# Kernel optimization log

Measured on AMD Instinct MI355X. Metric: run time of the kernel, lower is better.

## Reference

```python
import jax, jax.numpy as jnp
import numpy as np

DIM = 1024
NUM_HEAVY = 1024
N_ITERS = 50
EPS = 1.0
FETCH_K_RATIO = 9.0 / 8.0


def rms_norm(x, gamma):
    # F.normalize(x, dim=-1) * sqrt(d) * gamma
    norm = jnp.maximum(jnp.linalg.norm(x, axis=-1, keepdims=True), 1e-12)
    return (x / norm) * (x.shape[-1] ** 0.5) * gamma


def feed_forward(x, gamma, w1, b1, w2, b2):
    h = jax.nn.gelu(rms_norm(x, gamma) @ w1 + b1, approximate=False)
    return h @ w2 + b2


def coor_descent(s, k, n_iters, eps):
    # Wright et al. coordinate descent routing scores (eps_decay=1 -> constant eps)
    logk = jnp.log(jnp.asarray(k, dtype=s.dtype))

    def step(ab, _):
        a, b = ab
        sb = (s + b) / eps
        a = eps * (logk - jax.scipy.special.logsumexp(sb, axis=-1, keepdims=True))
        b = -jax.nn.relu(s + a)
        return (a, b), None

    a0 = jnp.zeros_like(s[..., :1])
    b0 = -s
    (a, b), _ = jax.lax.scan(step, (a0, b0), None, length=n_iters)
    return jnp.exp((s + a + b) / eps)


def setup_inputs() -> dict:
    key = jax.random.key(0)
    ks = jax.random.split(key, 8)
    b, n, d = 4, 8192, DIM
    dl, dh = int(d * 0.5), d * 4
    u = lambda k, shape, fan_in: jax.random.uniform(k, shape, jnp.float32, -1.0, 1.0) / np.sqrt(fan_in)
    return {
        "x": jax.random.normal(ks[0], (b, n, d), jnp.float32),
        "routing_token": jax.random.normal(ks[1], (d,), jnp.float32),
        "light_gamma": jnp.ones((d,), jnp.float32),
        "light_w1": u(ks[2], (d, dl), d),
        "light_b1": jnp.zeros((dl,), jnp.float32),
        "light_w2": u(ks[3], (dl, d), dl),
        "light_b2": jnp.zeros((d,), jnp.float32),
        "heavy_gamma": jnp.ones((d,), jnp.float32),
        "heavy_w1": u(ks[4], (d, dh), d),
        "heavy_b1": jnp.zeros((dh,), jnp.float32),
        "heavy_w2": u(ks[5], (dh, d), dh),
        "heavy_b2": jnp.zeros((d,), jnp.float32),
    }


def reference(x, routing_token, light_gamma, light_w1, light_b1, light_w2, light_b2,
              heavy_gamma, heavy_w1, heavy_b1, heavy_w2, heavy_b2):
    b, n, d = x.shape
    # light branch over all tokens
    light_out = feed_forward(x, light_gamma, light_w1, light_b1, light_w2, light_b2)

    # coordinate-descent router (single routing token)
    s = jnp.einsum('bnd,d->bn', x, routing_token)
    effective_k = min(NUM_HEAVY * FETCH_K_RATIO, n)
    scores = coor_descent(s, effective_k, N_ITERS, EPS)
    sel_scores, sel_idx = jax.lax.top_k(scores, NUM_HEAVY)  # [b, k]
    # straight-through: forward value 1.0, gradient flows through sel_scores
    sel_scores = sel_scores + jax.lax.stop_gradient(1.0 - sel_scores)

    # gather -> heavy FFN -> scale -> scatter back
    routed = jnp.take_along_axis(x, sel_idx[..., None], axis=1)  # [b, k, d]
    routed_out = feed_forward(routed, heavy_gamma, heavy_w1, heavy_b1, heavy_w2, heavy_b2)
    routed_out = routed_out * sel_scores[..., None]
    batch_idx = jnp.arange(b)[:, None]
    heavy_out = jnp.zeros_like(x).at[batch_idx, sel_idx].set(routed_out)

    return light_out + heavy_out
```

## Files before the change

kernel.cpp:

```cpp
#include <hip/hip_runtime.h>
#include <hip/hip_bf16.h>
#include <math.h>

#define DIMD   1024
#define NBATCH 4
#define NSEQ   8192
#define NTOK   (NBATCH * NSEQ)
#define NHEAVY 1024
#define NSEL   (NBATCH * NHEAVY)
#define DLIGHT 512
#define DHEAVY 4096
#define NITERS 50
#define BK     64

typedef __attribute__((ext_vector_type(8))) short short8;
typedef __attribute__((ext_vector_type(4))) float f32x4;
typedef __attribute__((ext_vector_type(4))) unsigned short u16x4;

__device__ __forceinline__ unsigned short f2bf(float f) {
    __hip_bfloat16 h = __float2bfloat16(f);
    union { __hip_bfloat16 h; unsigned short u; } cvt;
    cvt.h = h;
    return cvt.u;
}

__device__ __forceinline__ float bf2f(unsigned short u) {
    return __uint_as_float((unsigned)u << 16);
}

__device__ __forceinline__ float gelu_fast(float x) {
    float ax = fabsf(x) * 0.7071067811865475f;
    float t = 1.0f / fmaf(0.3275911f, ax, 1.0f);
    float p = fmaf(t, 1.061405429f, -1.453152027f);
    p = fmaf(t, p, 1.421413741f);
    p = fmaf(t, p, -0.284496736f);
    p = fmaf(t, p, 0.254829592f);
    p = p * t;
    float e = __expf(-ax * ax);
    float erf_abs = fmaf(-p, e, 1.0f);
    float erf = copysignf(erf_abs, x);
    return 0.5f * x * (1.0f + erf);
}

__device__ __forceinline__ void gload_lds16(const void* g, void* l) {
    __builtin_amdgcn_global_load_lds(
        (const __attribute__((address_space(1))) void*)g,
        (__attribute__((address_space(3))) void*)l,
        16, 0, 0);
}

__global__ __launch_bounds__(256) void fused_init(
    const float* __restrict__ lw1, const float* __restrict__ lw2,
    const float* __restrict__ hw1, const float* __restrict__ hw2,
    const float* __restrict__ lgamma, const float* __restrict__ hgamma,
    short* __restrict__ wl1t, short* __restrict__ wl2t,
    short* __restrict__ wh1t, short* __restrict__ wh2t,
    const float* __restrict__ x, const float* __restrict__ rt,
    unsigned short* __restrict__ xb, float* __restrict__ sc,
    double* __restrict__ s_out) {
    __shared__ float tile[32][33];
    __shared__ float red[4];
    __shared__ double redd[4];
    int b = blockIdx.x;
    int tid = threadIdx.x;

    const float* cin = nullptr; short* cout = nullptr; const float* cg = nullptr;
    int cK = 0, cN = 0, cnx = 0, cb = 0;
    if (b < 512)        { cin = lw1; cout = wl1t; cg = lgamma; cK = DIMD;   cN = DLIGHT; cnx = 16;  cb = b; }
    else if (b < 1024)  { cin = lw2; cout = wl2t; cg = nullptr; cK = DLIGHT; cN = DIMD;  cnx = 32;  cb = b - 512; }
    else if (b < 5120)  { cin = hw1; cout = wh1t; cg = hgamma; cK = DIMD;   cN = DHEAVY; cnx = 128; cb = b - 1024; }
    else if (b < 9216)  { cin = hw2; cout = wh2t; cg = nullptr; cK = DHEAVY; cN = DIMD;  cnx = 32;  cb = b - 5120; }

    if (cin) {
        int n0 = (cb % cnx) * 32, k0 = (cb / cnx) * 32;
        int tx = tid & 31, ty = tid >> 5;
        #pragma unroll
        for (int j = 0; j < 4; j++) {
            int k = k0 + ty + 8 * j;
            float g = cg ? cg[k] : 1.0f;
            tile[ty + 8 * j][tx] = cin[(size_t)k * cN + (n0 + tx)] * g;
        }
        __syncthreads();
        #pragma unroll
        for (int j = 0; j < 4; j++)
            cout[(size_t)(n0 + ty + 8 * j) * cK + (k0 + tx)] =
                (short)f2bf(tile[tx][ty + 8 * j]);
        return;
    }

    int t = b - 9216;
    const float4* xr = (const float4*)(x + (size_t)t * DIMD);
    float4 v = xr[tid];
    ushort4 pk;
    pk.x = f2bf(v.x); pk.y = f2bf(v.y); pk.z = f2bf(v.z); pk.w = f2bf(v.w);
    ((ushort4*)(xb + (size_t)t * DIMD))[tid] = pk;

    float ss = v.x * v.x + v.y * v.y + v.z * v.z + v.w * v.w;
    float4 rv = ((const float4*)rt)[tid];
    double sd = (double)v.x * rv.x + (double)v.y * rv.y + (double)v.z * rv.z + (double)v.w * rv.w;
    #pragma unroll
    for (int off = 32; off > 0; off >>= 1) {
        ss += __shfl_down(ss, off);
        sd += __shfl_down(sd, off);
    }
    if ((tid & 63) == 0) { red[tid >> 6] = ss; redd[tid >> 6] = sd; }
    __syncthreads();
    if (tid == 0) {
        s_out[t] = redd[0] + redd[1] + redd[2] + redd[3];
        float tot = red[0] + red[1] + red[2] + red[3];
        sc[t] = 32.0f / fmaxf(sqrtf(tot), 1e-12f);
    }
}

__global__ void descent_kern(const double* __restrict__ s, double* __restrict__ a_out) {
    int r = blockIdx.x, tid = threadIdx.x;
    const double* sr = s + (size_t)r * NSEQ;
    double es[8];
    #pragma unroll
    for (int i = 0; i < 8; i++) es[i] = exp(sr[tid + i * 1024]);
    __shared__ double red[2][16];
    const double Kk = 1152.0;
    double ea = exp(log(Kk) - log((double)NSEQ));
    for (int it = 1; it < NITERS; it++) {
        double loc = 0.0;
        #pragma unroll
        for (int i = 0; i < 8; i++) {
            double p = es[i] * ea;
            loc += (p < 1.0 ? p : 1.0);
        }
        #pragma unroll
        for (int off = 32; off > 0; off >>= 1) loc += __shfl_down(loc, off);
        int pb = it & 1;
        if ((tid & 63) == 0) red[pb][tid >> 6] = loc;
        __syncthreads();
        double S = 0.0;
        #pragma unroll
        for (int i = 0; i < 16; i++) S += red[pb][i];
        ea = ea * (Kk / S);
    }
    if (tid == 0) a_out[r] = log(ea);
}

__global__ void select_kern(const double* __restrict__ s, const double* __restrict__ a_arr,
                            int* __restrict__ sel, int* __restrict__ inv) {
    int r = blockIdx.x, l = threadIdx.x;
    const double* sr = s + (size_t)r * NSEQ;
    double a = a_arr[r];
    __shared__ double sw[NSEQ];
    int cnt = 0;
    for (int base = 0; base < NSEQ; base += 64) {
        int idx = base + l;
        double v = sr[idx];
        bool sat = (v + a) >= 0.0;
        sw[idx] = sat ? -1.0e300 : v;
        unsigned long long m = __ballot(sat);
        int pre = __popcll(m & ((1ull << l) - 1ull));
        if (sat) {
            int slot = cnt + pre;
            if (slot < NHEAVY) {
                sel[r * NHEAVY + slot] = r * NSEQ + idx;
                inv[r * NSEQ + idx] = r * NHEAVY + slot;
            }
        }
        cnt += (int)__popcll(m);
    }
    __syncthreads();
    for (int slot = cnt; slot < NHEAVY; slot++) {
        double best = -1.0e301; int bidx = NSEQ;
        for (int i = 0; i < NSEQ / 64; i++) {
            int idx = i * 64 + l;
            double v = sw[idx];
            if (v > best) { best = v; bidx = idx; }
        }
        #pragma unroll
        for (int off = 32; off > 0; off >>= 1) {
            double ov = __shfl_down(best, off);
            int oi = __shfl_down(bidx, off);
            if (ov > best || (ov == best && oi < bidx)) { best = ov; bidx = oi; }
        }
        bidx = __shfl(bidx, 0);
        if (l == 0) {
            sel[r * NHEAVY + slot] = r * NSEQ + bidx;
            inv[r * NSEQ + bidx] = r * NHEAVY + slot;
            sw[bidx] = -1.0e300;
        }
        __syncthreads();
    }
}

__global__ __launch_bounds__(256) void reduce_hv_kern(
    const unsigned short* __restrict__ phb, const float* __restrict__ hb2,
    float* __restrict__ hv, int nsk) {
    int h = blockIdx.x;
    int c0 = threadIdx.x * 4;
    f32x4 acc = *reinterpret_cast<const f32x4*>(hb2 + c0);
    for (int j = 0; j < nsk; j++) {
        u16x4 p = *reinterpret_cast<const u16x4*>(phb + ((size_t)j * NSEL + h) * DIMD + c0);
        #pragma unroll
        for (int rg = 0; rg < 4; rg++) acc[rg] += bf2f(p[rg]);
    }
    *reinterpret_cast<f32x4*>(hv + (size_t)h * DIMD + c0) = acc;
}

template <int EPI, bool GATHER>
__global__ __launch_bounds__(512) void gemm256(
    const short* __restrict__ A, const short* __restrict__ Bt,
    const float* __restrict__ bias,
    const float* __restrict__ sc, const int* __restrict__ sel,
    const int* __restrict__ inv, const float* __restrict__ hv,
    float* __restrict__ outf, __hip_bfloat16* __restrict__ outb,
    int M, int N, int K) {
    __shared__ alignas(16) short As[2][2][128 * 64];
    __shared__ alignas(16) short Bs[2][2][128 * 64];

    int nx = gridDim.x, ny = gridDim.y;
    int nwg = nx * ny * gridDim.z;
    int id = ((int)blockIdx.z * ny + blockIdx.y) * nx + blockIdx.x;
    if ((nwg & 7) == 0) id = (id & 7) * (nwg >> 3) + (id >> 3);
    int bxi = id % nx; int rem = id / nx;
    int byi = rem % ny; int bz = rem / ny;
    int klen = K / (int)gridDim.z, k0base = bz * klen;
    int bn0 = bxi * 256, bm0 = byi * 256;

    int tid = threadIdx.x;
    int l = tid & 63, w = tid >> 6;
    int wr = w >> 2, wc = w & 3;

    f32x4 zero = {0.f, 0.f, 0.f, 0.f};
    f32x4 acc[8][4];
    #pragma unroll
    for (int i = 0; i < 8; i++)
        #pragma unroll
        for (int j = 0; j < 4; j++) acc[i][j] = zero;

    const short* aSrc[2][2];
    const short* bSrc[2][2];
    #pragma unroll
    for (int h = 0; h < 2; h++)
        #pragma unroll
        for (int j = 0; j < 2; j++) {
            int p = j * 8192 + tid * 16;
            int o = p ^ (((p >> 7) & 7) << 4);
            int lrow = o >> 7, colb = o & 127;
            int agrow = bm0 + h * 128 + lrow;
            int garow = GATHER ? sel[agrow] : agrow;
            aSrc[h][j] = A + (size_t)garow * K + (colb >> 1);
            bSrc[h][j] = Bt + (size_t)(bn0 + h * 128 + lrow) * K + (colb >> 1);
        }

    auto stageA = [&](int b, int h, int kof) {
        #pragma unroll
        for (int j = 0; j < 2; j++)
            gload_lds16(aSrc[h][j] + kof, &As[b][h][j * 4096 + w * 512]);
    };
    auto stageB = [&](int b, int h, int kof) {
        #pragma unroll
        for (int j = 0; j < 2; j++)
            gload_lds16(bSrc[h][j] + kof, &Bs[b][h][j * 4096 + w * 512]);
    };

    int nt = klen / BK;
    stageA(0, 0, k0base); stageA(0, 1, k0base);
    stageB(0, 0, k0base); stageB(0, 1, k0base);
    if (nt > 1) {
        stageB(1, 0, k0base + BK); stageB(1, 1, k0base + BK);
        asm volatile("s_waitcnt vmcnt(4)" ::: "memory");
    } else {
        asm volatile("s_waitcnt vmcnt(0)" ::: "memory");
    }
    __builtin_amdgcn_s_barrier();

    const int lr = l & 15;
    const int swz = (lr & 7) << 4;
    const int rbase = lr * 128;
    const int colk[2] = { (((l >> 4) * 16)) ^ swz, (((l >> 4) * 16) + 64) ^ swz };

    short8 bfr[4][2];
    for (int t = 0; t < nt; ++t) {
        int d = t & 1;
        const char* aHalf = (const char*)(&As[d][wr][0]);
        const char* bHalf = (const char*)(&Bs[d][wc >> 1][0]) + (wc & 1) * 8192;
        #pragma unroll
        for (int q = 0; q < 4; q++) {
            if (q == 0) {
                #pragma unroll
                for (int ni = 0; ni < 4; ni++)
                    #pragma unroll
                    for (int kk = 0; kk < 2; kk++)
                        bfr[ni][kk] = *reinterpret_cast<const short8*>(bHalf + rbase + ni * 2048 + colk[kk]);
            }
            short8 afr[2][2];
            #pragma unroll
            for (int m2 = 0; m2 < 2; m2++)
                #pragma unroll
                for (int kk = 0; kk < 2; kk++)
                    afr[m2][kk] = *reinterpret_cast<const short8*>(aHalf + rbase + (q * 2 + m2) * 2048 + colk[kk]);
            if (q == 0 && t + 1 < nt) stageA(d ^ 1, 0, k0base + (t + 1) * BK);
            else if (q == 1 && t + 1 < nt) stageA(d ^ 1, 1, k0base + (t + 1) * BK);
            else if (q == 2 && t + 2 < nt) stageB(d, 0, k0base + (t + 2) * BK);
            else if (q == 3 && t + 2 < nt) stageB(d, 1, k0base + (t + 2) * BK);
            if (q == 3) {
                if (t + 2 < nt) asm volatile("s_waitcnt vmcnt(4)" ::: "memory");
                else            asm volatile("s_waitcnt vmcnt(0)" ::: "memory");
            }
            __builtin_amdgcn_s_barrier();
            asm volatile("s_waitcnt lgkmcnt(0)" ::: "memory");
            __builtin_amdgcn_sched_barrier(0);
            __builtin_amdgcn_s_setprio(1);
            #pragma unroll
            for (int m2 = 0; m2 < 2; m2++)
                #pragma unroll
                for (int ni = 0; ni < 4; ni++)
                    #pragma unroll
                    for (int kk = 0; kk < 2; kk++)
                        acc[q * 2 + m2][ni] = __builtin_amdgcn_mfma_f32_16x16x32_bf16(
                            bfr[ni][kk], afr[m2][kk], acc[q * 2 + m2][ni], 0, 0, 0);
            __builtin_amdgcn_s_setprio(0);
            __builtin_amdgcn_s_barrier();
        }
    }

    int orow0 = bm0 + wr * 128, ocol0 = bn0 + wc * 64;
    const int lq = (l >> 4) * 4;
    #pragma unroll
    for (int mi = 0; mi < 8; mi++) {
        int row = orow0 + mi * 16 + lr;
        float scv = 0.0f;
        int iv = -1;
        if (EPI == 0) scv = sc[GATHER ? sel[row] : row];
        if (EPI == 3) iv = inv[row];
        #pragma unroll
        for (int ni = 0; ni < 4; ni++) {
            int c0 = ocol0 + ni * 16 + lq;
            if (EPI == 0) {
                f32x4 bv = *reinterpret_cast<const f32x4*>(bias + c0);
                u16x4 pk;
                #pragma unroll
                for (int rg = 0; rg < 4; rg++)
                    pk[rg] = f2bf(gelu_fast(fmaf(scv, acc[mi][ni][rg], bv[rg])));
                *reinterpret_cast<u16x4*>((unsigned short*)outb + (size_t)row * N + c0) = pk;
            } else if (EPI == 2) {
                u16x4 pk;
                #pragma unroll
                for (int rg = 0; rg < 4; rg++) pk[rg] = f2bf(acc[mi][ni][rg]);
                *reinterpret_cast<u16x4*>((unsigned short*)outb + ((size_t)bz * M + row) * (size_t)N + c0) = pk;
            } else {
                f32x4 bv = *reinterpret_cast<const f32x4*>(bias + c0);
                f32x4 v = acc[mi][ni] + bv;
                if (iv >= 0) {
                    f32x4 hvv = *reinterpret_cast<const f32x4*>(hv + (size_t)iv * DIMD + c0);
                    v = v + hvv;
                }
                *reinterpret_cast<f32x4*>(outf + (size_t)row * N + c0) = v;
            }
        }
    }
}

extern "C" void kernel_launch(void* const* d_in, const int* in_sizes, int n_in,
                              void* d_out, int out_size, void* d_ws, size_t ws_size,
                              hipStream_t stream) {
    (void)in_sizes; (void)n_in; (void)out_size;
    const float* x      = (const float*)d_in[0];
    const float* rt     = (const float*)d_in[1];
    const float* lgamma = (const float*)d_in[2];
    const float* lw1    = (const float*)d_in[3];
    const float* lb1    = (const float*)d_in[4];
    const float* lw2    = (const float*)d_in[5];
    const float* lb2    = (const float*)d_in[6];
    const float* hgamma = (const float*)d_in[7];
    const float* hw1    = (const float*)d_in[8];
    const float* hb1    = (const float*)d_in[9];
    const float* hw2    = (const float*)d_in[10];
    const float* hb2    = (const float*)d_in[11];
    float* out = (float*)d_out;

    auto rnd = [](size_t b) { return (b + 255) & ~(size_t)255; };
    size_t fixed = rnd(NTOK * sizeof(double))
                 + rnd(256)
                 + rnd(NSEL * sizeof(int))
                 + rnd(NTOK * sizeof(int))
                 + rnd(NTOK * sizeof(float))
                 + rnd((size_t)DLIGHT * DIMD * 2)
                 + rnd((size_t)DIMD * DLIGHT * 2)
                 + rnd((size_t)DHEAVY * DIMD * 2)
                 + rnd((size_t)DIMD * DHEAVY * 2)
                 + rnd((size_t)NTOK * DIMD * 2)
                 + rnd((size_t)NSEL * DHEAVY * 2)
                 + rnd((size_t)NSEL * DIMD * 4);
    int nsk = 4;
    while (nsk > 1 && fixed + rnd((size_t)nsk * NSEL * DIMD * 2) > ws_size) nsk >>= 1;

    char* base = (char*)d_ws;
    size_t off = 0;
    auto alloc = [&](size_t bytes) -> void* {
        void* p = base + off;
        off += rnd(bytes);
        return p;
    };
    double* s     = (double*)alloc(NTOK * sizeof(double));
    double* a_arr = (double*)alloc(256);
    int*    sel   = (int*)alloc(NSEL * sizeof(int));
    int*    inv   = (int*)alloc(NTOK * sizeof(int));
    float*  sc    = (float*)alloc(NTOK * sizeof(float));
    short*  wl1t  = (short*)alloc((size_t)DLIGHT * DIMD * 2);
    short*  wl2t  = (short*)alloc((size_t)DIMD * DLIGHT * 2);
    short*  wh1t  = (short*)alloc((size_t)DHEAVY * DIMD * 2);
    short*  wh2t  = (short*)alloc((size_t)DIMD * DHEAVY * 2);
    short*  xb    = (short*)alloc((size_t)NTOK * DIMD * 2);
    short*  hh    = (short*)alloc((size_t)NSEL * DHEAVY * 2);
    float*  hv    = (float*)alloc((size_t)NSEL * DIMD * 4);
    short*  hl    = hh;
    short*  phb   = (short*)alloc((size_t)nsk * NSEL * DIMD * 2);

    hipMemsetAsync(inv, 0xFF, NTOK * sizeof(int), stream);

    fused_init<<<9216 + NTOK, 256, 0, stream>>>(
        lw1, lw2, hw1, hw2, lgamma, hgamma,
        wl1t, wl2t, wh1t, wh2t,
        x, rt, (unsigned short*)xb, sc, s);

    descent_kern<<<NBATCH, 1024, 0, stream>>>(s, a_arr);
    select_kern<<<NBATCH, 64, 0, stream>>>(s, a_arr, sel, inv);

    gemm256<0, true><<<dim3(DHEAVY / 256, NSEL / 256), 512, 0, stream>>>(
        xb, wh1t, hb1, sc, sel, nullptr, nullptr,
        nullptr, (__hip_bfloat16*)hh, NSEL, DHEAVY, DIMD);
    gemm256<2, false><<<dim3(DIMD / 256, NSEL / 256, nsk), 512, 0, stream>>>(
        hh, wh2t, nullptr, nullptr, nullptr, nullptr, nullptr,
        nullptr, (__hip_bfloat16*)phb, NSEL, DIMD, DHEAVY);
    reduce_hv_kern<<<NSEL, 256, 0, stream>>>((const unsigned short*)phb, hb2, hv, nsk);

    gemm256<0, false><<<dim3(DLIGHT / 256, NTOK / 256), 512, 0, stream>>>(
        xb, wl1t, lb1, sc, nullptr, nullptr, nullptr,
        nullptr, (__hip_bfloat16*)hl, NTOK, DLIGHT, DIMD);
    gemm256<3, false><<<dim3(DIMD / 256, NTOK / 256), 512, 0, stream>>>(
        hl, wl2t, lb2, nullptr, nullptr, inv, hv,
        out, nullptr, NTOK, DIMD, DLIGHT);
}
```

Baseline: 357.8 us.

## Overlap serial coordinate-descent router with light FFN first GEMM in one launch

Replaces the standalone 4-block descent kernel with a combined kernel whose first 4 blocks run the router iterations while the remaining 1024 blocks compute the light-branch first GEMM (128x128 tiles, GELU epilogue). The latency-bound 50-iteration descent, which used only 4 blocks, should then hide behind useful GEMM work. The light hidden buffer moves to its own allocation instead of aliasing the heavy hidden buffer, and the final output store becomes nontemporal. Risks: the smaller 128-tile GEMM may be less efficient than the 256-tile version, the descent blocks now use 256 threads with 32 values each, and the workspace grows.

```diff
diff --git a/kernel.cpp b/kernel.cpp
--- a/kernel.cpp
+++ b/kernel.cpp
@@ -112,33 +112,129 @@
     }
 }
 
-__global__ void descent_kern(const double* __restrict__ s, double* __restrict__ a_out) {
-    int r = blockIdx.x, tid = threadIdx.x;
-    const double* sr = s + (size_t)r * NSEQ;
-    double es[8];
-    #pragma unroll
-    for (int i = 0; i < 8; i++) es[i] = exp(sr[tid + i * 1024]);
-    __shared__ double red[2][16];
-    const double Kk = 1152.0;
-    double ea = exp(log(Kk) - log((double)NSEQ));
-    for (int it = 1; it < NITERS; it++) {
-        double loc = 0.0;
-        #pragma unroll
-        for (int i = 0; i < 8; i++) {
-            double p = es[i] * ea;
-            loc += (p < 1.0 ? p : 1.0);
-        }
-        #pragma unroll
-        for (int off = 32; off > 0; off >>= 1) loc += __shfl_down(loc, off);
-        int pb = it & 1;
-        if ((tid & 63) == 0) red[pb][tid >> 6] = loc;
-        __syncthreads();
-        double S = 0.0;
-        #pragma unroll
-        for (int i = 0; i < 16; i++) S += red[pb][i];
-        ea = ea * (Kk / S);
-    }
-    if (tid == 0) a_out[r] = log(ea);
+__global__ __launch_bounds__(256) void mega_kern(
+    const double* __restrict__ s, double* __restrict__ a_out,
+    const short* __restrict__ A, const short* __restrict__ Bt,
+    const float* __restrict__ bias, const float* __restrict__ sc,
+    __hip_bfloat16* __restrict__ outb) {
+    __shared__ alignas(16) short As[2][128 * 64];
+    __shared__ alignas(16) short Bs[2][128 * 64];
+    __shared__ double redd[2][4];
+    int tid = threadIdx.x;
+
+    if (blockIdx.x < 4) {
+        int r = blockIdx.x;
+        int l = tid & 63, w = tid >> 6;
+        const double* sr = s + (size_t)r * NSEQ;
+        double es[32];
+        #pragma unroll
+        for (int i = 0; i < 32; i++) es[i] = exp(sr[tid + i * 256]);
+        const double Kk = 1152.0;
+        double ea = exp(log(Kk) - log((double)NSEQ));
+        for (int it = 1; it < NITERS; it++) {
+            double loc = 0.0;
+            #pragma unroll
+            for (int i = 0; i < 32; i++) {
+                double p = es[i] * ea;
+                loc += (p < 1.0 ? p : 1.0);
+            }
+            #pragma unroll
+            for (int off = 32; off > 0; off >>= 1) loc += __shfl_down(loc, off);
+            int pb = it & 1;
+            if (l == 0) redd[pb][w] = loc;
+            __syncthreads();
+            double S = redd[pb][0] + redd[pb][1] + redd[pb][2] + redd[pb][3];
+            ea = ea * (Kk / S);
+        }
+        if (tid == 0) a_out[r] = log(ea);
+        return;
+    }
+
+    const int N = DLIGHT, K = DIMD;
+    int gid = blockIdx.x - 4;
+    int id = (gid & 7) * (1024 >> 3) + (gid >> 3);
+    int nx = N / 128;
+    int bxi = id % nx, byi = id / nx;
+    int l = tid & 63, w = tid >> 6;
+    int wr = w >> 1, wc = w & 1;
+    int bn0 = bxi * 128, bm0 = byi * 128;
+
+    f32x4 zero = {0.f, 0.f, 0.f, 0.f};
+    f32x4 acc[4][4];
+    #pragma unroll
+    for (int i = 0; i < 4; i++)
+        #pragma unroll
+        for (int j = 0; j < 4; j++) acc[i][j] = zero;
+
+    const int lrow = l & 15, lk = (l >> 4) * 8;
+    int srow = tid >> 3, scol = (tid & 7) * 8;
+    const short* AgC[4];
+    const short* BgC[4];
+    #pragma unroll
+    for (int c = 0; c < 4; c++) {
+        AgC[c] = A + (size_t)(bm0 + srow + c * 32) * K + scol;
+        BgC[c] = Bt + (size_t)(bn0 + srow + c * 32) * K + scol;
+    }
+    const int sbase = (tid & ~63) * 8;
+
+    auto stage = [&](int b, int k0) {
+        #pragma unroll
+        for (int c = 0; c < 4; c++) {
+            gload_lds16(AgC[c] + k0, &As[b][sbase + c * 2048]);
+            gload_lds16(BgC[c] + k0, &Bs[b][sbase + c * 2048]);
+        }
+    };
+
+    int nt = K / 64;
+    stage(0, 0);
+    for (int t = 0; t < nt; ++t) {
+        int cur = t & 1;
+        if (t + 1 < nt) {
+            stage(cur ^ 1, (t + 1) * 64);
+            asm volatile("s_waitcnt vmcnt(8)" ::: "memory");
+        } else {
+            asm volatile("s_waitcnt vmcnt(0)" ::: "memory");
+        }
+        __builtin_amdgcn_s_barrier();
+        asm volatile("" ::: "memory");
+        #pragma unroll
+        for (int kk = 0; kk < 2; kk++) {
+            short8 af[4], bf[4];
+            #pragma unroll
+            for (int i = 0; i < 4; i++) {
+                af[i] = *reinterpret_cast<const short8*>(&As[cur][(wr * 64 + i * 16 + lrow) * 64 + kk * 32 + lk]);
+                bf[i] = *reinterpret_cast<const short8*>(&Bs[cur][(wc * 64 + i * 16 + lrow) * 64 + kk * 32 + lk]);
+            }
+            #pragma unroll
+            for (int mi = 0; mi < 4; mi++)
+                #pragma unroll
+                for (int ni = 0; ni < 4; ni++)
+                    acc[mi][ni] = __builtin_amdgcn_mfma_f32_16x16x32_bf16(bf[ni], af[mi], acc[mi][ni], 0, 0, 0);
+        }
+        if (t + 1 < nt) {
+            asm volatile("" ::: "memory");
+            __builtin_amdgcn_s_barrier();
+            asm volatile("" ::: "memory");
+        }
+    }
+
+    int orow0 = bm0 + wr * 64, ocol0 = bn0 + wc * 64;
+    const int lr = l & 15, lq = (l >> 4) * 4;
+    #pragma unroll
+    for (int mi = 0; mi < 4; mi++) {
+        int row = orow0 + mi * 16 + lr;
+        float scv = sc[row];
+        #pragma unroll
+        for (int ni = 0; ni < 4; ni++) {
+            int c0 = ocol0 + ni * 16 + lq;
+            f32x4 bv = *reinterpret_cast<const f32x4*>(bias + c0);
+            u16x4 pk;
+            #pragma unroll
+            for (int rg = 0; rg < 4; rg++)
+                pk[rg] = f2bf(gelu_fast(fmaf(scv, acc[mi][ni][rg], bv[rg])));
+            *reinterpret_cast<u16x4*>((unsigned short*)outb + (size_t)row * N + c0) = pk;
+        }
+    }
 }
 
 __global__ void select_kern(const double* __restrict__ s, const double* __restrict__ a_arr,
@@ -351,7 +447,7 @@
                     f32x4 hvv = *reinterpret_cast<const f32x4*>(hv + (size_t)iv * DIMD + c0);
                     v = v + hvv;
                 }
-                *reinterpret_cast<f32x4*>(outf + (size_t)row * N + c0) = v;
+                __builtin_nontemporal_store(v, reinterpret_cast<f32x4*>(outf + (size_t)row * N + c0));
             }
         }
     }
@@ -387,6 +483,7 @@
                  + rnd((size_t)DIMD * DHEAVY * 2)
                  + rnd((size_t)NTOK * DIMD * 2)
                  + rnd((size_t)NSEL * DHEAVY * 2)
+                 + rnd((size_t)NTOK * DLIGHT * 2)
                  + rnd((size_t)NSEL * DIMD * 4);
     int nsk = 4;
     while (nsk > 1 && fixed + rnd((size_t)nsk * NSEL * DIMD * 2) > ws_size) nsk >>= 1;
@@ -409,8 +506,8 @@
     short*  wh2t  = (short*)alloc((size_t)DIMD * DHEAVY * 2);
     short*  xb    = (short*)alloc((size_t)NTOK * DIMD * 2);
     short*  hh    = (short*)alloc((size_t)NSEL * DHEAVY * 2);
+    short*  hl    = (short*)alloc((size_t)NTOK * DLIGHT * 2);
     float*  hv    = (float*)alloc((size_t)NSEL * DIMD * 4);
-    short*  hl    = hh;
     short*  phb   = (short*)alloc((size_t)nsk * NSEL * DIMD * 2);
 
     hipMemsetAsync(inv, 0xFF, NTOK * sizeof(int), stream);
@@ -420,7 +517,9 @@
         wl1t, wl2t, wh1t, wh2t,
         x, rt, (unsigned short*)xb, sc, s);
 
-    descent_kern<<<NBATCH, 1024, 0, stream>>>(s, a_arr);
+    mega_kern<<<4 + 1024, 256, 0, stream>>>(
+        s, a_arr, xb, wl1t, lb1, sc, (__hip_bfloat16*)hl);
+
     select_kern<<<NBATCH, 64, 0, stream>>>(s, a_arr, sel, inv);
 
     gemm256<0, true><<<dim3(DHEAVY / 256, NSEL / 256), 512, 0, stream>>>(
@@ -431,9 +530,6 @@
         nullptr, (__hip_bfloat16*)phb, NSEL, DIMD, DHEAVY);
     reduce_hv_kern<<<NSEL, 256, 0, stream>>>((const unsigned short*)phb, hb2, hv, nsk);
 
-    gemm256<0, false><<<dim3(DLIGHT / 256, NTOK / 256), 512, 0, stream>>>(
-        xb, wl1t, lb1, sc, nullptr, nullptr, nullptr,
-        nullptr, (__hip_bfloat16*)hl, NTOK, DLIGHT, DIMD);
     gemm256<3, false><<<dim3(DIMD / 256, NTOK / 256), 512, 0, stream>>>(
         hl, wl2t, lb2, nullptr, nullptr, inv, hv,
         out, nullptr, NTOK, DIMD, DLIGHT);
```

Measured after the change: 340.7 us. -4.8%, faster.
